# Kernel optimization log

Hardware: AMD Instinct MI355X
Metric: run time of the kernel (lower is better)

The kernel has to match this reference:

```python
import jax, jax.numpy as jnp
import numpy as np

NUM_HEADS = 32


def setup_inputs() -> dict:
    key = jax.random.key(0)
    k1, k2, k3 = jax.random.split(key, 3)
    B, C = 8192, 4096
    x = jax.random.normal(k1, (B, C), dtype=jnp.float32)
    w_qkv = jax.random.normal(k2, (3 * C, C), dtype=jnp.float32) * (C ** -0.5)
    w_proj = jax.random.normal(k3, (C, C), dtype=jnp.float32) * (C ** -0.5)
    b_proj = jnp.zeros((C,), dtype=jnp.float32)
    return {"x": x, "w_qkv": w_qkv, "w_proj": w_proj, "b_proj": b_proj}


def reference(x, w_qkv, w_proj, b_proj):
    B, C = x.shape
    H = NUM_HEADS
    hd = C // H
    scale = hd ** -0.5
    # qkv projection: (B, 3C) -> (B, 3, H, hd)
    qkv = (x @ w_qkv.T).reshape(B, 3, H, hd)
    q, k, v = qkv[:, 0], qkv[:, 1], qkv[:, 2]  # each (B, H, hd)
    # tiny per-row attention over heads: scores (B, H, H)
    attn = jax.nn.softmax(jnp.einsum("bhd,bgd->bhg", q, k) * scale, axis=-1)
    out = jnp.einsum("bhg,bgd->bhd", attn, v)  # (B, H, hd)
    # faithful to torch: transpose(1,2) then reshape -> head-dim-major flatten
    out = out.transpose(0, 2, 1).reshape(B, C)
    return out @ w_proj.T + b_proj
```

## Files before the change

kernel.cpp:

```cpp
#include <hip/hip_runtime.h>
#include <hip/hip_bf16.h>
#include <stdint.h>

typedef __attribute__((ext_vector_type(8))) short bf16x8;
typedef __attribute__((ext_vector_type(4))) float f32x4;
typedef __hip_bfloat16 bf16;

typedef const __attribute__((address_space(1))) void* gas_ptr;
typedef __attribute__((address_space(3))) void* las_ptr;

__device__ __forceinline__ void async_load16(const bf16* g, bf16* l) {
  __builtin_amdgcn_global_load_lds((gas_ptr)g, (las_ptr)l, 16, 0, 0);
}

__global__ __launch_bounds__(256) void cvt_kernel(
    const float* __restrict__ in, bf16* __restrict__ out, int n8) {
  int i = blockIdx.x * blockDim.x + threadIdx.x;
  if (i >= n8) return;
  const float4* p = (const float4*)in;
  float4 a = p[2 * i], b = p[2 * i + 1];
  union { bf16x8 v; bf16 h[8]; } u;
  u.h[0] = __float2bfloat16(a.x); u.h[1] = __float2bfloat16(a.y);
  u.h[2] = __float2bfloat16(a.z); u.h[3] = __float2bfloat16(a.w);
  u.h[4] = __float2bfloat16(b.x); u.h[5] = __float2bfloat16(b.y);
  u.h[6] = __float2bfloat16(b.z); u.h[7] = __float2bfloat16(b.w);
  ((bf16x8*)out)[i] = u.v;
}

template <int BIAS, typename OutT>
__global__ __launch_bounds__(256, 2) void gemm_bt_kernel(
    const bf16* __restrict__ A, const bf16* __restrict__ B,
    const float* __restrict__ bias, OutT* __restrict__ C,
    int M, int N, int K) {
  __shared__ __attribute__((aligned(16))) bf16 As[128 * 32];
  __shared__ __attribute__((aligned(16))) bf16 Bs[128 * 32];

  const int tid  = threadIdx.x;
  const int lane = tid & 63;
  const int wv   = tid >> 6;
  const int wm   = wv & 1;
  const int wn   = wv >> 1;
  const int quad = lane >> 4;
  const int l15  = lane & 15;
  const int m0 = blockIdx.y * 128;
  const int n0 = blockIdx.x * 128;

  f32x4 acc[4][4];
  const f32x4 zero = {0.f, 0.f, 0.f, 0.f};
#pragma unroll
  for (int i = 0; i < 4; ++i)
#pragma unroll
    for (int j = 0; j < 4; ++j) acc[i][j] = zero;

  for (int k0 = 0; k0 < K; k0 += 32) {
#pragma unroll
    for (int call = 0; call < 2; ++call) {
      const int c = wv * 128 + call * 64 + lane;
      const int r = c >> 2;
      const int jj = c & 3;
      const size_t ga = (size_t)(m0 + r) * K + k0 + jj * 8;
      const size_t gb = (size_t)(n0 + r) * K + k0 + jj * 8;
      async_load16(A + ga, As + (wv * 128 + call * 64) * 8);
      async_load16(B + gb, Bs + (wv * 128 + call * 64) * 8);
    }
    __syncthreads();

    bf16x8 af[4], bfr[4];
#pragma unroll
    for (int t = 0; t < 4; ++t) {
      af[t]  = *(const bf16x8*)(As + (wm * 64 + t * 16 + l15) * 32 + quad * 8);
      bfr[t] = *(const bf16x8*)(Bs + (wn * 64 + t * 16 + l15) * 32 + quad * 8);
    }
#pragma unroll
    for (int tm = 0; tm < 4; ++tm)
#pragma unroll
      for (int tn = 0; tn < 4; ++tn)
        acc[tm][tn] = __builtin_amdgcn_mfma_f32_16x16x32_bf16(
            af[tm], bfr[tn], acc[tm][tn], 0, 0, 0);
    __syncthreads();
  }

#pragma unroll
  for (int tm = 0; tm < 4; ++tm) {
    const int row0 = m0 + wm * 64 + tm * 16 + quad * 4;
#pragma unroll
    for (int tn = 0; tn < 4; ++tn) {
      const int col = n0 + wn * 64 + tn * 16 + l15;
      float bv = 0.f;
      if (BIAS) bv = bias[col];
#pragma unroll
      for (int i = 0; i < 4; ++i) {
        float v = acc[tm][tn][i] + bv;
        if constexpr (sizeof(OutT) == 2)
          C[(size_t)(row0 + i) * N + col] = __float2bfloat16(v);
        else
          C[(size_t)(row0 + i) * N + col] = v;
      }
    }
  }
}

__global__ __launch_bounds__(256) void attn_kernel(
    const bf16* __restrict__ qkv, bf16* __restrict__ out) {
  const int b = blockIdx.x;
  const int tid = threadIdx.x;
  __shared__ uint32_t sQKV[3 * 32 * 65];
  __shared__ float S[32][33];

  const uint32_t* src = (const uint32_t*)(qkv + (size_t)b * 12288);
#pragma unroll
  for (int i = 0; i < 24; ++i) {
    int c = tid + i * 256;
    int sec = c >> 11;
    int cc = c & 2047;
    int row = cc >> 6;
    int col = cc & 63;
    sQKV[sec * 2080 + row * 65 + col] = src[c];
  }
  __syncthreads();

  const float scale = 0.088388347648318447f;
#pragma unroll
  for (int i = 0; i < 4; ++i) {
    int p = tid + i * 256;
    int h = p >> 5;
    int g = p & 31;
    const __hip_bfloat162* qr = (const __hip_bfloat162*)(sQKV + h * 65);
    const __hip_bfloat162* kr = (const __hip_bfloat162*)(sQKV + 2080 + g * 65);
    float acc = 0.f;
#pragma unroll
    for (int d = 0; d < 64; ++d) {
      float2 qf = __bfloat1622float2(qr[d]);
      float2 kf = __bfloat1622float2(kr[d]);
      acc = fmaf(qf.x, kf.x, acc);
      acc = fmaf(qf.y, kf.y, acc);
    }
    S[h][g] = acc * scale;
  }
  __syncthreads();

  if (tid < 32) {
    float m = -1e30f;
#pragma unroll
    for (int g = 0; g < 32; ++g) m = fmaxf(m, S[tid][g]);
    float sum = 0.f;
#pragma unroll
    for (int g = 0; g < 32; ++g) {
      float e = __expf(S[tid][g] - m);
      S[tid][g] = e;
      sum += e;
    }
    float inv = 1.f / sum;
#pragma unroll
    for (int g = 0; g < 32; ++g) S[tid][g] *= inv;
  }
  __syncthreads();

  const bf16* V = (const bf16*)(sQKV + 2 * 2080);
  bf16* orow = out + (size_t)b * 4096;
#pragma unroll
  for (int i = 0; i < 16; ++i) {
    int c = tid + i * 256;
    int d = c >> 5;
    int h = c & 31;
    float acc = 0.f;
#pragma unroll
    for (int g = 0; g < 32; ++g)
      acc = fmaf(S[h][g], __bfloat162float(V[g * 130 + d]), acc);
    orow[c] = __float2bfloat16(acc);
  }
}

extern "C" void kernel_launch(void* const* d_in, const int* in_sizes, int n_in,
                              void* d_out, int out_size, void* d_ws, size_t ws_size,
                              hipStream_t stream) {
  const float* x      = (const float*)d_in[0];
  const float* w_qkv  = (const float*)d_in[1];
  const float* w_proj = (const float*)d_in[2];
  const float* b_proj = (const float*)d_in[3];
  float* out = (float*)d_out;

  const int C = in_sizes[3];
  const int B = in_sizes[0] / C;

  bf16* xb    = (bf16*)d_ws;
  bf16* wqb   = xb + (size_t)B * C;
  bf16* qkvb  = wqb + (size_t)3 * C * C;
  bf16* attnb = xb;
  bf16* wpb   = wqb;

  const int nx = B * C / 8, nwq = 3 * C * C / 8, nwp = C * C / 8;
  cvt_kernel<<<(nx + 255) / 256, 256, 0, stream>>>(x, xb, nx);
  cvt_kernel<<<(nwq + 255) / 256, 256, 0, stream>>>(w_qkv, wqb, nwq);

  gemm_bt_kernel<0, bf16><<<dim3(3 * C / 128, B / 128), 256, 0, stream>>>(
      xb, wqb, nullptr, qkvb, B, 3 * C, C);
  attn_kernel<<<B, 256, 0, stream>>>(qkvb, attnb);
  cvt_kernel<<<(nwp + 255) / 256, 256, 0, stream>>>(w_proj, wpb, nwp);
  gemm_bt_kernel<1, float><<<dim3(C / 128, B / 128), 256, 0, stream>>>(
      attnb, wpb, b_proj, out, B, C, C);
}
```

Measured before the change: 1.907 ms.

## Replace 128x128 GEMM with pipelined 256x256 double-buffered swizzled MFMA kernel

Replaces the simple 128x128-tile bf16 GEMM with a 512-thread, 256x256-tile kernel. It stages K=64 slabs into double-buffered LDS with an XOR swizzle and interleaves half-tile async global->LDS loads with quadrant MFMA groups, using explicit vmcnt/lgkmcnt waits, barriers and setprio. A remapped workgroup order is meant to improve L2 locality. The goal is to hide global load latency and raise arithmetic intensity per LDS byte, at the cost of heavy register use (128 accumulator floats), a large LDS footprint, and hand-tuned wait counts that could be fragile.

Result: faster. 1.758 ms (-7.8%).

```diff
diff --git a/kernel.cpp b/kernel.cpp
--- a/kernel.cpp
+++ b/kernel.cpp
@@ -12,6 +12,16 @@
 __device__ __forceinline__ void async_load16(const bf16* g, bf16* l) {
   __builtin_amdgcn_global_load_lds((gas_ptr)g, (las_ptr)l, 16, 0, 0);
 }
+
+#define BAR()                                   \
+  do {                                          \
+    asm volatile("" ::: "memory");              \
+    __builtin_amdgcn_s_barrier();               \
+    asm volatile("" ::: "memory");              \
+  } while (0)
+#define LGKM0() asm volatile("s_waitcnt lgkmcnt(0)" ::: "memory")
+#define VMCNT6() asm volatile("s_waitcnt vmcnt(6)" ::: "memory")
+#define VMCNT0() asm volatile("s_waitcnt vmcnt(0)" ::: "memory")
 
 __global__ __launch_bounds__(256) void cvt_kernel(
     const float* __restrict__ in, bf16* __restrict__ out, int n8) {
@@ -27,70 +37,186 @@
   ((bf16x8*)out)[i] = u.v;
 }
 
+
+__device__ __forceinline__ bf16x8 ld_frag(const bf16* buf, int rl, int j) {
+  return *(const bf16x8*)(buf + rl * 64 + ((j ^ (rl & 7)) << 3));
+}
+
+__device__ __forceinline__ void stage_halfA(const bf16* __restrict__ G,
+                                            int row0, int K, int kt, bf16* buf,
+                                            int r0, int wv, int lane) {
+#pragma unroll
+  for (int c = 0; c < 2; ++c) {
+    const int sl = c * 512 + wv * 64 + lane;
+    const int rl = r0 + (sl >> 3);
+    const int j = (sl & 7) ^ (rl & 7);
+    const int grow = ((rl >> 6) & 1) * 128 + ((rl >> 7) & 1) * 64 + (rl & 63);
+    async_load16(G + (size_t)(row0 + grow) * K + kt + j * 8,
+                 buf + r0 * 64 + c * 4096 + wv * 512);
+  }
+}
+
+__device__ __forceinline__ void stage_halfB(const bf16* __restrict__ G,
+                                            int row0, int K, int kt, bf16* buf,
+                                            int r0, int wv, int lane) {
+#pragma unroll
+  for (int c = 0; c < 2; ++c) {
+    const int sl = c * 512 + wv * 64 + lane;
+    const int rl = r0 + (sl >> 3);
+    const int j = (sl & 7) ^ (rl & 7);
+    const int grow = ((rl >> 5) & 3) * 64 + ((rl >> 7) & 1) * 32 + (rl & 31);
+    async_load16(G + (size_t)(row0 + grow) * K + kt + j * 8,
+                 buf + r0 * 64 + c * 4096 + wv * 512);
+  }
+}
+
+#define READ_A(DST, BUF, QM)                                                  \
+  {                                                                           \
+    _Pragma("unroll") for (int tm = 0; tm < 4; ++tm) {                        \
+      _Pragma("unroll") for (int ks = 0; ks < 2; ++ks) {                      \
+        DST[tm * 2 + ks] =                                                    \
+            ld_frag(BUF, (QM) * 128 + wm * 64 + tm * 16 + l15, ks * 4 + quad);\
+      }                                                                       \
+    }                                                                         \
+  }
+
+#define READ_B(DST, BUF, QN)                                                  \
+  {                                                                           \
+    _Pragma("unroll") for (int tn = 0; tn < 2; ++tn) {                        \
+      _Pragma("unroll") for (int ks = 0; ks < 2; ++ks) {                      \
+        DST[tn * 2 + ks] =                                                    \
+            ld_frag(BUF, (QN) * 128 + wn * 32 + tn * 16 + l15, ks * 4 + quad);\
+      }                                                                       \
+    }                                                                         \
+  }
+
+#define MFMA_Q(QM, QN, AF, BF)                                                \
+  {                                                                           \
+    __builtin_amdgcn_s_setprio(1);                                            \
+    _Pragma("unroll") for (int tm = 0; tm < 4; ++tm) {                        \
+      _Pragma("unroll") for (int tn = 0; tn < 2; ++tn) {                      \
+        _Pragma("unroll") for (int ks = 0; ks < 2; ++ks) {                    \
+          acc[(QM) * 4 + tm][(QN) * 2 + tn] =                                 \
+              __builtin_amdgcn_mfma_f32_16x16x32_bf16(                        \
+                  AF[tm * 2 + ks], BF[tn * 2 + ks],                           \
+                  acc[(QM) * 4 + tm][(QN) * 2 + tn], 0, 0, 0);                \
+        }                                                                     \
+      }                                                                       \
+    }                                                                         \
+    __builtin_amdgcn_s_setprio(0);                                            \
+  }
+
 template <int BIAS, typename OutT>
-__global__ __launch_bounds__(256, 2) void gemm_bt_kernel(
+__global__ __launch_bounds__(512, 2) void gemm256_kernel(
     const bf16* __restrict__ A, const bf16* __restrict__ B,
     const float* __restrict__ bias, OutT* __restrict__ C,
     int M, int N, int K) {
-  __shared__ __attribute__((aligned(16))) bf16 As[128 * 32];
-  __shared__ __attribute__((aligned(16))) bf16 Bs[128 * 32];
-
-  const int tid  = threadIdx.x;
+  __shared__ __attribute__((aligned(16))) bf16 sA[2][256 * 64];
+  __shared__ __attribute__((aligned(16))) bf16 sB[2][256 * 64];
+
+  const int tid = threadIdx.x;
   const int lane = tid & 63;
-  const int wv   = tid >> 6;
-  const int wm   = wv & 1;
-  const int wn   = wv >> 1;
+  const int wv = tid >> 6;
+  const int wm = wv >> 2;
+  const int wn = wv & 3;
   const int quad = lane >> 4;
-  const int l15  = lane & 15;
-  const int m0 = blockIdx.y * 128;
-  const int n0 = blockIdx.x * 128;
-
-  f32x4 acc[4][4];
+  const int l15 = lane & 15;
+
+  const int nwg = gridDim.x;
+  const int bid = blockIdx.x;
+  const int wg = (bid & 7) * (nwg >> 3) + (bid >> 3);
+  const int nby = M >> 8;
+  const int by = wg % nby;
+  const int bx = wg / nby;
+  const int m0 = by * 256;
+  const int n0 = bx * 256;
+
+  const int NT = K >> 6;
+  const int klast = (NT - 1) << 6;
+
+  f32x4 acc[8][4];
   const f32x4 zero = {0.f, 0.f, 0.f, 0.f};
 #pragma unroll
-  for (int i = 0; i < 4; ++i)
+  for (int i = 0; i < 8; ++i)
 #pragma unroll
     for (int j = 0; j < 4; ++j) acc[i][j] = zero;
 
-  for (int k0 = 0; k0 < K; k0 += 32) {
-#pragma unroll
-    for (int call = 0; call < 2; ++call) {
-      const int c = wv * 128 + call * 64 + lane;
-      const int r = c >> 2;
-      const int jj = c & 3;
-      const size_t ga = (size_t)(m0 + r) * K + k0 + jj * 8;
-      const size_t gb = (size_t)(n0 + r) * K + k0 + jj * 8;
-      async_load16(A + ga, As + (wv * 128 + call * 64) * 8);
-      async_load16(B + gb, Bs + (wv * 128 + call * 64) * 8);
-    }
-    __syncthreads();
-
-    bf16x8 af[4], bfr[4];
-#pragma unroll
-    for (int t = 0; t < 4; ++t) {
-      af[t]  = *(const bf16x8*)(As + (wm * 64 + t * 16 + l15) * 32 + quad * 8);
-      bfr[t] = *(const bf16x8*)(Bs + (wn * 64 + t * 16 + l15) * 32 + quad * 8);
-    }
-#pragma unroll
-    for (int tm = 0; tm < 4; ++tm)
-#pragma unroll
-      for (int tn = 0; tn < 4; ++tn)
-        acc[tm][tn] = __builtin_amdgcn_mfma_f32_16x16x32_bf16(
-            af[tm], bfr[tn], acc[tm][tn], 0, 0, 0);
-    __syncthreads();
-  }
-
-#pragma unroll
-  for (int tm = 0; tm < 4; ++tm) {
-    const int row0 = m0 + wm * 64 + tm * 16 + quad * 4;
-#pragma unroll
-    for (int tn = 0; tn < 4; ++tn) {
-      const int col = n0 + wn * 64 + tn * 16 + l15;
+  stage_halfA(A, m0, K, 0, sA[0], 0, wv, lane);
+  stage_halfB(B, n0, K, 0, sB[0], 0, wv, lane);
+  stage_halfB(B, n0, K, 0, sB[0], 128, wv, lane);
+  stage_halfA(A, m0, K, 0, sA[0], 128, wv, lane);
+  stage_halfA(A, m0, K, 64, sA[1], 0, wv, lane);
+  stage_halfB(B, n0, K, 64, sB[1], 0, wv, lane);
+  stage_halfB(B, n0, K, 64, sB[1], 128, wv, lane);
+  VMCNT6();
+  BAR();
+
+  for (int it = 0; it < (NT >> 1); ++it) {
+    const int kt0 = it << 7;
+    const int kt1 = kt0 + 64;
+    const int ks0 = (kt0 + 128 < klast) ? kt0 + 128 : klast;
+    const int ks1 = (kt0 + 192 < klast) ? kt0 + 192 : klast;
+
+    bf16x8 a0f[8], a1f[8], b0f[4], b1f[4];
+
+    READ_A(a0f, sA[0], 0);
+    READ_B(b0f, sB[0], 0);
+    stage_halfA(A, m0, K, kt1, sA[1], 128, wv, lane);
+    BAR(); LGKM0();
+    MFMA_Q(0, 0, a0f, b0f);
+    BAR();
+    READ_B(b1f, sB[0], 1);
+    stage_halfA(A, m0, K, ks0, sA[0], 0, wv, lane);
+    BAR(); LGKM0();
+    MFMA_Q(0, 1, a0f, b1f);
+    BAR();
+    READ_A(a1f, sA[0], 1);
+    stage_halfB(B, n0, K, ks0, sB[0], 0, wv, lane);
+    BAR(); LGKM0();
+    MFMA_Q(1, 0, a1f, b0f);
+    BAR();
+    stage_halfB(B, n0, K, ks0, sB[0], 128, wv, lane);
+    BAR(); LGKM0();
+    MFMA_Q(1, 1, a1f, b1f);
+    VMCNT6();
+    BAR();
+
+    READ_A(a0f, sA[1], 0);
+    READ_B(b0f, sB[1], 0);
+    stage_halfA(A, m0, K, ks0, sA[0], 128, wv, lane);
+    BAR(); LGKM0();
+    MFMA_Q(0, 0, a0f, b0f);
+    BAR();
+    READ_B(b1f, sB[1], 1);
+    stage_halfA(A, m0, K, ks1, sA[1], 0, wv, lane);
+    BAR(); LGKM0();
+    MFMA_Q(0, 1, a0f, b1f);
+    BAR();
+    READ_A(a1f, sA[1], 1);
+    stage_halfB(B, n0, K, ks1, sB[1], 0, wv, lane);
+    BAR(); LGKM0();
+    MFMA_Q(1, 0, a1f, b0f);
+    BAR();
+    stage_halfB(B, n0, K, ks1, sB[1], 128, wv, lane);
+    BAR(); LGKM0();
+    MFMA_Q(1, 1, a1f, b1f);
+    VMCNT6();
+    BAR();
+  }
+
+  VMCNT0();
+
+#pragma unroll
+  for (int mf = 0; mf < 8; ++mf) {
+    const int row0 = m0 + wm * 128 + (mf >> 2) * 64 + (mf & 3) * 16 + quad * 4;
+#pragma unroll
+    for (int nf = 0; nf < 4; ++nf) {
+      const int col = n0 + wn * 64 + (nf >> 1) * 32 + (nf & 1) * 16 + l15;
       float bv = 0.f;
       if (BIAS) bv = bias[col];
 #pragma unroll
       for (int i = 0; i < 4; ++i) {
-        float v = acc[tm][tn][i] + bv;
+        float v = acc[mf][nf][i] + bv;
         if constexpr (sizeof(OutT) == 2)
           C[(size_t)(row0 + i) * N + col] = __float2bfloat16(v);
         else
@@ -193,10 +319,10 @@
   cvt_kernel<<<(nx + 255) / 256, 256, 0, stream>>>(x, xb, nx);
   cvt_kernel<<<(nwq + 255) / 256, 256, 0, stream>>>(w_qkv, wqb, nwq);
 
-  gemm_bt_kernel<0, bf16><<<dim3(3 * C / 128, B / 128), 256, 0, stream>>>(
+  gemm256_kernel<0, bf16><<<(3 * C / 256) * (B / 256), 512, 0, stream>>>(
       xb, wqb, nullptr, qkvb, B, 3 * C, C);
   attn_kernel<<<B, 256, 0, stream>>>(qkvb, attnb);
   cvt_kernel<<<(nwp + 255) / 256, 256, 0, stream>>>(w_proj, wpb, nwp);
-  gemm_bt_kernel<1, float><<<dim3(C / 128, B / 128), 256, 0, stream>>>(
+  gemm256_kernel<1, float><<<(C / 256) * (B / 256), 512, 0, stream>>>(
       attnb, wpb, b_proj, out, B, C, C);
 }
```
